# Optimization experiments

Measured on AMD Instinct MI355X. Metric: run time of the kernel, lower is better.

Reference implementation:

```python
import jax, jax.numpy as jnp
import numpy as np

EPS = 1e-05      # self.eps
BETA = -1.0      # self.beta
THRESH = 0.0     # self.thresh
NUM_BASIS = 5
D_PARAMS = 16_777_216  # flattened network parameter count


def setup_inputs() -> dict:
    key = jax.random.key(0)
    k1, k2, k3 = jax.random.split(key, 3)
    m, Dp = NUM_BASIS, D_PARAMS
    # K = (1/L) * dkdxdy @ dkdxdy^T is a Gram matrix -> build a PSD 5x5
    A = jax.random.normal(k1, (m, m), dtype=jnp.float32)
    K = (A @ A.T) / m
    # T = dkdx @ noise / (L * noise_std): [num_basis, n_params]
    T = 0.01 * jax.random.normal(k2, (m, Dp), dtype=jnp.float32)
    # g: flattened loss gradient, [n_params]
    g = jax.random.normal(k3, (Dp,), dtype=jnp.float32)
    return {"K": K, "T": T, "g": g}


def reference(K, T, g):
    # --- compute_natural_gradient ---
    # torch.svd: K = U diag(s) V^T ; jnp.linalg.svd gives u, s, vh with vh = V^T
    u, s, vh = jnp.linalg.svd(K)
    mask = s > THRESH                              # pseudo_inverse mask, [m] bool
    ss_inv = jnp.where(mask, 1.0 / jnp.where(mask, s, 1.0), 0.0)
    ss_inv = jnp.sqrt(ss_inv)
    # torch: vv = einsum('i,ji->ij', ss_inv, V) == diag(ss_inv) @ V^T
    W = ss_inv[:, None] * vh                       # [m, m]
    Tt = W @ T                                     # whitened T, [m, D]

    # --- make_system (with_diag_mat == 1) ---
    Dv = 1.0 / (jnp.sqrt(jnp.sum(Tt * Tt, axis=0)) + 1e-08)   # [D]
    cond_g = Tt @ (Dv * g)                         # [m]
    P = mask.astype(Tt.dtype)                      # one on kept singular dirs
    G = (Tt * Dv) @ Tt.T + EPS * jnp.diag(P)       # [m, m]

    # cholesky_solve on SPD G == linear solve (same math, robust form)
    cond_g = jnp.linalg.solve(G, cond_g)           # [m]
    cond_g = Tt.T @ cond_g                         # einsum('md,m->d'), [D]
    cond_g = (g - BETA * cond_g) / EPS
    return Dv * cond_g
```

## Files before the change

### kernel.cpp

```cpp
#include <hip/hip_runtime.h>
#include <math.h>


#define WS_W  0
#define WS_P  25
#define WS_CG 32
#define WS_G  40
#define WS_X  64

typedef float fvec4 __attribute__((ext_vector_type(4)));

__global__ void kwng_prep(const float* __restrict__ K, float* __restrict__ ws) {
    if (blockIdx.x != 0 || threadIdx.x != 0) return;
    double a[5][5], V[5][5];
    for (int i = 0; i < 5; i++)
        for (int j = 0; j < 5; j++) {
            a[i][j] = (double)K[i * 5 + j];
            V[i][j] = (i == j) ? 1.0 : 0.0;
        }
    for (int sweep = 0; sweep < 30; sweep++) {
        double off = 0.0;
        for (int p = 0; p < 5; p++)
            for (int q = p + 1; q < 5; q++) off += a[p][q] * a[p][q];
        if (off < 1e-26) break;
        for (int p = 0; p < 5; p++) {
            for (int q = p + 1; q < 5; q++) {
                double apq = a[p][q];
                if (fabs(apq) < 1e-300) continue;
                double tau = (a[q][q] - a[p][p]) / (2.0 * apq);
                double t = ((tau >= 0.0) ? 1.0 : -1.0) /
                           (fabs(tau) + sqrt(1.0 + tau * tau));
                double c = 1.0 / sqrt(1.0 + t * t);
                double s = t * c;
                for (int k = 0; k < 5; k++) {
                    double akp = a[k][p], akq = a[k][q];
                    a[k][p] = c * akp - s * akq;
                    a[k][q] = s * akp + c * akq;
                }
                for (int k = 0; k < 5; k++) {
                    double apk = a[p][k], aqk = a[q][k];
                    a[p][k] = c * apk - s * aqk;
                    a[q][k] = s * apk + c * aqk;
                }
                for (int k = 0; k < 5; k++) {
                    double vkp = V[k][p], vkq = V[k][q];
                    V[k][p] = c * vkp - s * vkq;
                    V[k][q] = s * vkp + c * vkq;
                }
            }
        }
    }
    for (int i = 0; i < 5; i++) {
        double si = a[i][i];
        int keep = (si > 0.0);
        double inv = keep ? 1.0 / sqrt(si) : 0.0;
        ws[WS_P + i] = keep ? 1.0f : 0.0f;
        for (int j = 0; j < 5; j++)
            ws[WS_W + i * 5 + j] = (float)(inv * V[j][i]);
    }
    for (int i = 0; i < 5; i++)  ws[WS_CG + i] = 0.0f;
    for (int i = 0; i < 15; i++) ws[WS_G + i] = 0.0f;
}

__device__ __forceinline__ void col_accum(const float W[25],
                                          float c0, float c1, float c2,
                                          float c3, float c4, float gc,
                                          float cg[5], float Gu[15]) {
    float tt[5];
#pragma unroll
    for (int i = 0; i < 5; i++)
        tt[i] = W[i * 5 + 0] * c0 + W[i * 5 + 1] * c1 + W[i * 5 + 2] * c2 +
                W[i * 5 + 3] * c3 + W[i * 5 + 4] * c4;
    float ss = tt[0] * tt[0] + tt[1] * tt[1] + tt[2] * tt[2] +
               tt[3] * tt[3] + tt[4] * tt[4];
    float dv = 1.0f / (sqrtf(ss) + 1e-8f);
    float dg = dv * gc;
#pragma unroll
    for (int i = 0; i < 5; i++) cg[i] += tt[i] * dg;
    int idx = 0;
#pragma unroll
    for (int i = 0; i < 5; i++) {
        float tdi = tt[i] * dv;
#pragma unroll
        for (int l = i; l < 5; l++) Gu[idx++] += tdi * tt[l];
    }
}

__device__ __forceinline__ float col_out(const float W[25], const float x[5],
                                         float c0, float c1, float c2,
                                         float c3, float c4, float gc) {
    float tt[5];
#pragma unroll
    for (int i = 0; i < 5; i++)
        tt[i] = W[i * 5 + 0] * c0 + W[i * 5 + 1] * c1 + W[i * 5 + 2] * c2 +
                W[i * 5 + 3] * c3 + W[i * 5 + 4] * c4;
    float ss = tt[0] * tt[0] + tt[1] * tt[1] + tt[2] * tt[2] +
               tt[3] * tt[3] + tt[4] * tt[4];
    float dv = 1.0f / (sqrtf(ss) + 1e-8f);
    float xc = tt[0] * x[0] + tt[1] * x[1] + tt[2] * x[2] +
               tt[3] * x[3] + tt[4] * x[4];
    return dv * (gc + xc) * (1.0f / 1e-5f);
}

__launch_bounds__(256)
__global__ void kwng_pass1(const float* __restrict__ T, const float* __restrict__ g,
                           float* __restrict__ ws, int D) {
    float W[25];
#pragma unroll
    for (int i = 0; i < 25; i++) W[i] = ws[WS_W + i];

    float cg[5] = {0, 0, 0, 0, 0};
    float Gu[15];
#pragma unroll
    for (int i = 0; i < 15; i++) Gu[i] = 0.0f;

    const int NV = D >> 2;
    const float4* T0 = (const float4*)T;
    const float4* T1 = (const float4*)(T + (size_t)D);
    const float4* T2 = (const float4*)(T + 2 * (size_t)D);
    const float4* T3 = (const float4*)(T + 3 * (size_t)D);
    const float4* T4 = (const float4*)(T + 4 * (size_t)D);
    const float4* G4 = (const float4*)g;

    int tid = blockIdx.x * blockDim.x + threadIdx.x;
    int stride = gridDim.x * blockDim.x;
    for (int v = tid; v < NV; v += stride) {
        float4 t0 = T0[v], t1 = T1[v], t2 = T2[v], t3 = T3[v], t4 = T4[v];
        float4 gv = G4[v];
        col_accum(W, t0.x, t1.x, t2.x, t3.x, t4.x, gv.x, cg, Gu);
        col_accum(W, t0.y, t1.y, t2.y, t3.y, t4.y, gv.y, cg, Gu);
        col_accum(W, t0.z, t1.z, t2.z, t3.z, t4.z, gv.z, cg, Gu);
        col_accum(W, t0.w, t1.w, t2.w, t3.w, t4.w, gv.w, cg, Gu);
    }

    __shared__ float red[4][20];
    float vals[20];
#pragma unroll
    for (int i = 0; i < 20; i++) {
        float v = (i < 5) ? cg[i] : Gu[i - 5];
#pragma unroll
        for (int off = 32; off > 0; off >>= 1) v += __shfl_down(v, off);
        vals[i] = v;
    }
    int lane = threadIdx.x & 63;
    int wid = threadIdx.x >> 6;
    if (lane == 0) {
#pragma unroll
        for (int i = 0; i < 20; i++) red[wid][i] = vals[i];
    }
    __syncthreads();
    if (threadIdx.x == 0) {
#pragma unroll
        for (int i = 0; i < 20; i++) {
            float s = red[0][i] + red[1][i] + red[2][i] + red[3][i];
            atomicAdd(&ws[(i < 5) ? (WS_CG + i) : (WS_G + i - 5)], s);
        }
    }
}

__global__ void kwng_solve(float* __restrict__ ws) {
    if (blockIdx.x != 0 || threadIdx.x != 0) return;
    double A[5][6];
    int idx = 0;
    for (int i = 0; i < 5; i++)
        for (int l = i; l < 5; l++) {
            double v = (double)ws[WS_G + idx++];
            A[i][l] = v;
            A[l][i] = v;
        }
    for (int i = 0; i < 5; i++)
        A[i][i] += 1e-5 * (double)ws[WS_P + i];
    for (int i = 0; i < 5; i++) A[i][5] = (double)ws[WS_CG + i];

    for (int k = 0; k < 5; k++) {
        int piv = k;
        for (int r = k + 1; r < 5; r++)
            if (fabs(A[r][k]) > fabs(A[piv][k])) piv = r;
        if (piv != k)
            for (int j = 0; j < 6; j++) {
                double tmp = A[k][j]; A[k][j] = A[piv][j]; A[piv][j] = tmp;
            }
        double d = A[k][k];
        double dinv = (d != 0.0) ? 1.0 / d : 0.0;
        for (int j = k; j < 6; j++) A[k][j] *= dinv;
        for (int r = 0; r < 5; r++) {
            if (r == k) continue;
            double f = A[r][k];
            for (int j = k; j < 6; j++) A[r][j] -= f * A[k][j];
        }
    }
    for (int i = 0; i < 5; i++) ws[WS_X + i] = (float)A[i][5];
}

__launch_bounds__(256)
__global__ void kwng_pass2(const float* __restrict__ T, const float* __restrict__ g,
                           const float* __restrict__ ws, float* __restrict__ out,
                           int D) {
    float W[25], x[5];
#pragma unroll
    for (int i = 0; i < 25; i++) W[i] = ws[WS_W + i];
#pragma unroll
    for (int i = 0; i < 5; i++) x[i] = ws[WS_X + i];

    const int NV = D >> 2;
    int bid = gridDim.x - 1 - blockIdx.x;
    int v = bid * blockDim.x + threadIdx.x;
    if (v >= NV) return;

    const float4* T0 = (const float4*)T;
    const float4* T1 = (const float4*)(T + (size_t)D);
    const float4* T2 = (const float4*)(T + 2 * (size_t)D);
    const float4* T3 = (const float4*)(T + 3 * (size_t)D);
    const float4* T4 = (const float4*)(T + 4 * (size_t)D);
    const float4* G4 = (const float4*)g;

    float4 t0 = T0[v], t1 = T1[v], t2 = T2[v], t3 = T3[v], t4 = T4[v];
    float4 gv = G4[v];
    fvec4 o;
    o.x = col_out(W, x, t0.x, t1.x, t2.x, t3.x, t4.x, gv.x);
    o.y = col_out(W, x, t0.y, t1.y, t2.y, t3.y, t4.y, gv.y);
    o.z = col_out(W, x, t0.z, t1.z, t2.z, t3.z, t4.z, gv.z);
    o.w = col_out(W, x, t0.w, t1.w, t2.w, t3.w, t4.w, gv.w);
    __builtin_nontemporal_store(o, ((fvec4*)out) + v);
}

extern "C" void kernel_launch(void* const* d_in, const int* in_sizes, int n_in,
                              void* d_out, int out_size, void* d_ws, size_t ws_size,
                              hipStream_t stream) {
    const float* K = (const float*)d_in[0];
    const float* T = (const float*)d_in[1];
    const float* g = (const float*)d_in[2];
    float* out = (float*)d_out;
    float* ws = (float*)d_ws;
    const int D = in_sizes[2];
    const int NV = D >> 2;

    kwng_prep<<<1, 1, 0, stream>>>(K, ws);

    kwng_pass1<<<2048, 256, 0, stream>>>(T, g, ws, D);

    kwng_solve<<<1, 1, 0, stream>>>(ws);

    int blocks2 = (NV + 255) / 256;
    kwng_pass2<<<blocks2, 256, 0, stream>>>(T, g, ws, out, D);
}
```

Measured before the change: 892.8 us.

## Stage T and g tiles into LDS via direct global-to-LDS loads in both passes

Both streaming passes now copy 512-float4 tiles of the five T rows and g into shared memory using the global_load_lds builtin, then compute from LDS between two barriers. Pass 2 moves from one block per 256 float4s to a persistent 2048-block grid-stride loop that walks tiles in reverse. The aim is to issue wide asynchronous loads without holding data in registers. The cost is extra barriers and LDS traffic, and with no double buffering the loads and compute inside a block do not overlap.

New measurement: 852.3 us. -4.5%, faster.

```diff
diff --git a/kernel.cpp b/kernel.cpp
--- a/kernel.cpp
+++ b/kernel.cpp
@@ -9,6 +9,16 @@
 #define WS_X  64
 
 typedef float fvec4 __attribute__((ext_vector_type(4)));
+
+#define TILE_F4   512
+#define ROW_BYTES 8192
+
+__device__ __forceinline__ void gload_lds16(const float* gsrc, void* ldsdst) {
+    __builtin_amdgcn_global_load_lds(
+        (const __attribute__((address_space(1))) unsigned int*)gsrc,
+        (__attribute__((address_space(3))) unsigned int*)ldsdst,
+        16, 0, 0);
+}
 
 __global__ void kwng_prep(const float* __restrict__ K, float* __restrict__ ws) {
     if (blockIdx.x != 0 || threadIdx.x != 0) return;
@@ -86,6 +96,16 @@
     }
 }
 
+__device__ __forceinline__ void col_accum4(const float W[25],
+                                           float4 t0, float4 t1, float4 t2,
+                                           float4 t3, float4 t4, float4 gv,
+                                           float cg[5], float Gu[15]) {
+    col_accum(W, t0.x, t1.x, t2.x, t3.x, t4.x, gv.x, cg, Gu);
+    col_accum(W, t0.y, t1.y, t2.y, t3.y, t4.y, gv.y, cg, Gu);
+    col_accum(W, t0.z, t1.z, t2.z, t3.z, t4.z, gv.z, cg, Gu);
+    col_accum(W, t0.w, t1.w, t2.w, t3.w, t4.w, gv.w, cg, Gu);
+}
+
 __device__ __forceinline__ float col_out(const float W[25], const float x[5],
                                          float c0, float c1, float c2,
                                          float c3, float c4, float gc) {
@@ -102,9 +122,38 @@
     return dv * (gc + xc) * (1.0f / 1e-5f);
 }
 
+__device__ __forceinline__ fvec4 col_out4(const float W[25], const float x[5],
+                                          float4 t0, float4 t1, float4 t2,
+                                          float4 t3, float4 t4, float4 gv) {
+    fvec4 o;
+    o.x = col_out(W, x, t0.x, t1.x, t2.x, t3.x, t4.x, gv.x);
+    o.y = col_out(W, x, t0.y, t1.y, t2.y, t3.y, t4.y, gv.y);
+    o.z = col_out(W, x, t0.z, t1.z, t2.z, t3.z, t4.z, gv.z);
+    o.w = col_out(W, x, t0.w, t1.w, t2.w, t3.w, t4.w, gv.w);
+    return o;
+}
+
+__device__ __forceinline__ void stage_tile(const float* __restrict__ T,
+                                           const float* __restrict__ g,
+                                           int D, size_t col0f, void* smem) {
+    int wid = (int)threadIdx.x >> 6;
+    int lane = (int)threadIdx.x & 63;
+#pragma unroll
+    for (int j = 0; j < 12; ++j) {
+        int u = wid * 12 + j;
+        int row = u >> 3;
+        int ko = u & 7;
+        const float* src = (row < 5) ? (T + (size_t)row * (size_t)D) : g;
+        src += col0f + (size_t)ko * 256 + (size_t)lane * 4;
+        gload_lds16(src, (char*)smem + row * ROW_BYTES + ko * 1024);
+    }
+}
+
 __launch_bounds__(256)
 __global__ void kwng_pass1(const float* __restrict__ T, const float* __restrict__ g,
                            float* __restrict__ ws, int D) {
+    __shared__ float4 smem4[6 * TILE_F4];
+
     float W[25];
 #pragma unroll
     for (int i = 0; i < 25; i++) W[i] = ws[WS_W + i];
@@ -115,35 +164,55 @@
     for (int i = 0; i < 15; i++) Gu[i] = 0.0f;
 
     const int NV = D >> 2;
-    const float4* T0 = (const float4*)T;
-    const float4* T1 = (const float4*)(T + (size_t)D);
-    const float4* T2 = (const float4*)(T + 2 * (size_t)D);
-    const float4* T3 = (const float4*)(T + 3 * (size_t)D);
-    const float4* T4 = (const float4*)(T + 4 * (size_t)D);
-    const float4* G4 = (const float4*)g;
-
-    int tid = blockIdx.x * blockDim.x + threadIdx.x;
-    int stride = gridDim.x * blockDim.x;
-    for (int v = tid; v < NV; v += stride) {
-        float4 t0 = T0[v], t1 = T1[v], t2 = T2[v], t3 = T3[v], t4 = T4[v];
-        float4 gv = G4[v];
-        col_accum(W, t0.x, t1.x, t2.x, t3.x, t4.x, gv.x, cg, Gu);
-        col_accum(W, t0.y, t1.y, t2.y, t3.y, t4.y, gv.y, cg, Gu);
-        col_accum(W, t0.z, t1.z, t2.z, t3.z, t4.z, gv.z, cg, Gu);
-        col_accum(W, t0.w, t1.w, t2.w, t3.w, t4.w, gv.w, cg, Gu);
+    const int ntiles = NV >> 9;
+
+    for (int tl = (int)blockIdx.x; tl < ntiles; tl += (int)gridDim.x) {
+        stage_tile(T, g, D, (size_t)tl * (TILE_F4 * 4), smem4);
+        __syncthreads();
+
+        int t0 = (int)threadIdx.x;
+        {
+            float4 r0 = smem4[0 * TILE_F4 + t0], r1 = smem4[1 * TILE_F4 + t0],
+                   r2 = smem4[2 * TILE_F4 + t0], r3 = smem4[3 * TILE_F4 + t0],
+                   r4 = smem4[4 * TILE_F4 + t0], rg = smem4[5 * TILE_F4 + t0];
+            col_accum4(W, r0, r1, r2, r3, r4, rg, cg, Gu);
+        }
+        {
+            int t1 = t0 + 256;
+            float4 r0 = smem4[0 * TILE_F4 + t1], r1 = smem4[1 * TILE_F4 + t1],
+                   r2 = smem4[2 * TILE_F4 + t1], r3 = smem4[3 * TILE_F4 + t1],
+                   r4 = smem4[4 * TILE_F4 + t1], rg = smem4[5 * TILE_F4 + t1];
+            col_accum4(W, r0, r1, r2, r3, r4, rg, cg, Gu);
+        }
+        __syncthreads();
+    }
+
+    int rem0 = ntiles << 9;
+    if ((int)blockIdx.x == 0) {
+        const float4* T0 = (const float4*)T;
+        const float4* T1 = (const float4*)(T + (size_t)D);
+        const float4* T2 = (const float4*)(T + 2 * (size_t)D);
+        const float4* T3 = (const float4*)(T + 3 * (size_t)D);
+        const float4* T4 = (const float4*)(T + 4 * (size_t)D);
+        const float4* G4 = (const float4*)g;
+        for (int v = rem0 + (int)threadIdx.x; v < NV; v += 256) {
+            float4 t0 = T0[v], t1 = T1[v], t2 = T2[v], t3 = T3[v], t4 = T4[v];
+            float4 gv = G4[v];
+            col_accum4(W, t0, t1, t2, t3, t4, gv, cg, Gu);
+        }
     }
 
     __shared__ float red[4][20];
     float vals[20];
 #pragma unroll
     for (int i = 0; i < 20; i++) {
-        float v = (i < 5) ? cg[i] : Gu[i - 5];
-#pragma unroll
-        for (int off = 32; off > 0; off >>= 1) v += __shfl_down(v, off);
-        vals[i] = v;
-    }
-    int lane = threadIdx.x & 63;
-    int wid = threadIdx.x >> 6;
+        float val = (i < 5) ? cg[i] : Gu[i - 5];
+#pragma unroll
+        for (int off = 32; off > 0; off >>= 1) val += __shfl_down(val, off);
+        vals[i] = val;
+    }
+    int lane = (int)threadIdx.x & 63;
+    int wid = (int)threadIdx.x >> 6;
     if (lane == 0) {
 #pragma unroll
         for (int i = 0; i < 20; i++) red[wid][i] = vals[i];
@@ -196,6 +265,8 @@
 __global__ void kwng_pass2(const float* __restrict__ T, const float* __restrict__ g,
                            const float* __restrict__ ws, float* __restrict__ out,
                            int D) {
+    __shared__ float4 smem4[6 * TILE_F4];
+
     float W[25], x[5];
 #pragma unroll
     for (int i = 0; i < 25; i++) W[i] = ws[WS_W + i];
@@ -203,25 +274,49 @@
     for (int i = 0; i < 5; i++) x[i] = ws[WS_X + i];
 
     const int NV = D >> 2;
-    int bid = gridDim.x - 1 - blockIdx.x;
-    int v = bid * blockDim.x + threadIdx.x;
-    if (v >= NV) return;
-
-    const float4* T0 = (const float4*)T;
-    const float4* T1 = (const float4*)(T + (size_t)D);
-    const float4* T2 = (const float4*)(T + 2 * (size_t)D);
-    const float4* T3 = (const float4*)(T + 3 * (size_t)D);
-    const float4* T4 = (const float4*)(T + 4 * (size_t)D);
-    const float4* G4 = (const float4*)g;
-
-    float4 t0 = T0[v], t1 = T1[v], t2 = T2[v], t3 = T3[v], t4 = T4[v];
-    float4 gv = G4[v];
-    fvec4 o;
-    o.x = col_out(W, x, t0.x, t1.x, t2.x, t3.x, t4.x, gv.x);
-    o.y = col_out(W, x, t0.y, t1.y, t2.y, t3.y, t4.y, gv.y);
-    o.z = col_out(W, x, t0.z, t1.z, t2.z, t3.z, t4.z, gv.z);
-    o.w = col_out(W, x, t0.w, t1.w, t2.w, t3.w, t4.w, gv.w);
-    __builtin_nontemporal_store(o, ((fvec4*)out) + v);
+    const int ntiles = NV >> 9;
+    fvec4* O4 = (fvec4*)out;
+
+    for (int tl0 = (int)blockIdx.x; tl0 < ntiles; tl0 += (int)gridDim.x) {
+        int tl = ntiles - 1 - tl0;
+        stage_tile(T, g, D, (size_t)tl * (TILE_F4 * 4), smem4);
+        __syncthreads();
+
+        int base = tl << 9;
+        int t0 = (int)threadIdx.x;
+        {
+            float4 r0 = smem4[0 * TILE_F4 + t0], r1 = smem4[1 * TILE_F4 + t0],
+                   r2 = smem4[2 * TILE_F4 + t0], r3 = smem4[3 * TILE_F4 + t0],
+                   r4 = smem4[4 * TILE_F4 + t0], rg = smem4[5 * TILE_F4 + t0];
+            __builtin_nontemporal_store(col_out4(W, x, r0, r1, r2, r3, r4, rg),
+                                        O4 + base + t0);
+        }
+        {
+            int t1 = t0 + 256;
+            float4 r0 = smem4[0 * TILE_F4 + t1], r1 = smem4[1 * TILE_F4 + t1],
+                   r2 = smem4[2 * TILE_F4 + t1], r3 = smem4[3 * TILE_F4 + t1],
+                   r4 = smem4[4 * TILE_F4 + t1], rg = smem4[5 * TILE_F4 + t1];
+            __builtin_nontemporal_store(col_out4(W, x, r0, r1, r2, r3, r4, rg),
+                                        O4 + base + t1);
+        }
+        __syncthreads();
+    }
+
+    int rem0 = ntiles << 9;
+    if ((int)blockIdx.x == 0) {
+        const float4* T0 = (const float4*)T;
+        const float4* T1 = (const float4*)(T + (size_t)D);
+        const float4* T2 = (const float4*)(T + 2 * (size_t)D);
+        const float4* T3 = (const float4*)(T + 3 * (size_t)D);
+        const float4* T4 = (const float4*)(T + 4 * (size_t)D);
+        const float4* G4 = (const float4*)g;
+        for (int v = rem0 + (int)threadIdx.x; v < NV; v += 256) {
+            float4 t0 = T0[v], t1 = T1[v], t2 = T2[v], t3 = T3[v], t4 = T4[v];
+            float4 gv = G4[v];
+            __builtin_nontemporal_store(col_out4(W, x, t0, t1, t2, t3, t4, gv),
+                                        O4 + v);
+        }
+    }
 }
 
 extern "C" void kernel_launch(void* const* d_in, const int* in_sizes, int n_in,
@@ -233,7 +328,6 @@
     float* out = (float*)d_out;
     float* ws = (float*)d_ws;
     const int D = in_sizes[2];
-    const int NV = D >> 2;
 
     kwng_prep<<<1, 1, 0, stream>>>(K, ws);
 
@@ -241,6 +335,5 @@
 
     kwng_solve<<<1, 1, 0, stream>>>(ws);
 
-    int blocks2 = (NV + 255) / 256;
-    kwng_pass2<<<blocks2, 256, 0, stream>>>(T, g, ws, out, D);
-}
+    kwng_pass2<<<2048, 256, 0, stream>>>(T, g, ws, out, D);
+}
```
